# Optimization experiments

Measured on AMD Instinct MI355X. Metric: run time of the kernel, lower is better.

Reference implementation:

```python
import jax, jax.numpy as jnp
import numpy as np

N_UP, N_DOWN, M, D, K, F, L, B = 16, 16, 4, 128, 64, 32, 3, 1024
N = N_UP + N_DOWN
H_W = 45  # round(sqrt(F*K)), hidden dim of the 2-layer w MLP
LOG2 = float(np.log(2.0))


def ssp(x):
    # shifted softplus activation used by deepqmc
    return jax.nn.softplus(x) - LOG2


def _pair_blocks(n_up, n_down):
    # replicate idx_perm(N,2) grouped by i, then idx_pair_spin partition
    n = n_up + n_down
    i = np.repeat(np.arange(n), n - 1)
    j = np.concatenate([np.concatenate([np.arange(k), np.arange(k + 1, n)]) for k in range(n)])
    blocks = []
    for mi, mj, ri, rj in [(True, True, n_up, max(n_up - 1, 0)),
                           (True, False, n_up, n_down),
                           (False, True, n_down, n_up),
                           (False, False, n_down, max(n_down - 1, 0))]:
        mask = ((i < n_up) == mi) & ((j < n_up) == mj)
        blocks.append((i[mask].reshape(ri, rj), j[mask].reshape(ri, rj)))
    return blocks

_BLOCKS = _pair_blocks(N_UP, N_DOWN)
_CHANS = [0, 1, 1, 0]  # same, anti, anti, same (w/g channel index; 2 = nuclear)


def setup_inputs() -> dict:
    key = jax.random.key(0)
    ks = jax.random.split(key, 12)
    s = 0.1
    return {
        'edges_elec': jax.random.normal(ks[0], (B, N, N, F), jnp.float32),
        'edges_nuc': jax.random.normal(ks[1], (B, N, M, F), jnp.float32),
        'X': jax.random.normal(ks[2], (1, D), jnp.float32) * s,
        'Y': jax.random.normal(ks[3], (M, K), jnp.float32) * s,
        'wW1': jax.random.normal(ks[4], (L, 3, H_W, F), jnp.float32) * s,
        'wb1': jax.random.normal(ks[5], (L, 3, H_W), jnp.float32) * s,
        'wW2': jax.random.normal(ks[6], (L, 3, K, H_W), jnp.float32) * s,
        'wb2': jax.random.normal(ks[7], (L, 3, K), jnp.float32) * s,
        'hW': jax.random.normal(ks[8], (L, K, D), jnp.float32) * s,
        'hb': jax.random.normal(ks[9], (L, K), jnp.float32) * s,
        'gW': jax.random.normal(ks[10], (L, 3, D, K), jnp.float32) * s,
        'gb': jax.random.normal(ks[11], (L, 3, D), jnp.float32) * s,
    }


def reference(edges_elec, edges_nuc, X, Y, wW1, wb1, wW2, wb2, hW, hb, gW, gb):
    def w_mlp(l, c, e):
        # 2-layer log-dim MLP: F -> H_W -> K with SSP in between
        return ssp(e @ wW1[l, c].T + wb1[l, c]) @ wW2[l, c].T + wb2[l, c]

    b = edges_nuc.shape[0]
    x = jnp.broadcast_to(X, (b, N, D))  # initial electron embeddings (n_up==n_down)
    for l in range(L):
        h = x @ hW[l].T + hb[l]  # shared h subnet: [b,N,K]
        zs = []
        for (ii, jj), c in zip(_BLOCKS, _CHANS):
            e = edges_elec[:, ii, jj, :]               # [b, ri, rj, F] gather
            msg = w_mlp(l, c, e) * h[:, jj, :]          # [b, ri, rj, K]
            zs.append(msg.sum(axis=-2))                 # segment-sum over j
        z_same = jnp.concatenate([zs[0], zs[3]], axis=-2)  # up then down
        z_anti = jnp.concatenate([zs[1], zs[2]], axis=-2)
        z_nuc = jnp.einsum('bnmk,mk->bnk', w_mlp(l, 2, edges_nuc), Y)
        update = (z_same @ gW[l, 0].T + gb[l, 0]
                  + z_anti @ gW[l, 1].T + gb[l, 1]
                  + z_nuc @ gW[l, 2].T + gb[l, 2])
        x = x + update  # resnet
    return x
```

## Files before the change

### kernel.cpp

```cpp
#include <hip/hip_runtime.h>
#include <math.h>

#define N_   32
#define NUP_ 16
#define M_   4
#define D_   128
#define K_   64
#define F_   32
#define H_   45
#define L_   3
#define LOG2_ 0.69314718055994530942f

typedef __attribute__((ext_vector_type(8))) short short8;
typedef __attribute__((ext_vector_type(4))) float float4v;

__device__ __forceinline__ float ssp(float v) {
    return __logf(fmaf(0.5f, __expf(v), 0.5f));
}

__device__ __forceinline__ unsigned short f2bf(float x) {
    unsigned int u = __float_as_uint(x);
    return (unsigned short)((u + 0x7FFFu + ((u >> 16) & 1u)) >> 16);
}

__device__ __forceinline__ unsigned int cvtpk(float x, float y) {
    unsigned int r;
    asm("v_cvt_pk_bf16_f32 %0, %1, %2" : "=v"(r) : "v"(x), "v"(y));
    return r;
}

__global__ __launch_bounds__(256) void prep_kernel(
    const float* __restrict__ wW1, const float* __restrict__ wb1_unused,
    const float* __restrict__ wW2, const float* __restrict__ wb2,
    const float* __restrict__ gW,  const float* __restrict__ hW,
    const float* __restrict__ gb,
    short* __restrict__ w1B, short* __restrict__ w2B,
    short* __restrict__ gB,  short* __restrict__ hB, float* __restrict__ gbs)
{
    int blk = blockIdx.x;
    int t = threadIdx.x;
    if (blk < 27) {
        int lc = blk / 3, nt = blk % 3;
        short* dst = w1B + (size_t)blk * 512;
        for (int idx = t; idx < 512; idx += 256) {
            int lane = idx >> 3, jj = idx & 7;
            int k = ((lane >> 4) << 3) + jj;
            int n = nt * 16 + (lane & 15);
            float v = (n < H_) ? wW1[((size_t)lc * H_ + n) * F_ + k] : 0.0f;
            dst[idx] = (short)f2bf(v);
        }
    } else if (blk < 99) {
        int b3 = blk - 27;
        int lc = b3 >> 3, rem = b3 & 7, ks = rem >> 2, nt = rem & 3;
        short* dst = w2B + (size_t)b3 * 512;
        for (int idx = t; idx < 512; idx += 256) {
            int lane = idx >> 3, jj = idx & 7;
            int p = ks * 32 + ((lane >> 4) << 3) + jj;
            int n = nt * 16 + (lane & 15);
            int q = (p & 31) >> 3, j = p & 7;
            float v;
            if (p < 32) {
                int u = (j >> 2) * 16 + q * 4 + (j & 3);
                v = wW2[((size_t)lc * K_ + n) * H_ + u];
            } else if (j < 4) {
                int u = 32 + q * 4 + j;
                v = (u < H_) ? wW2[((size_t)lc * K_ + n) * H_ + u] : 0.0f;
            } else if (p == 36) {
                v = wb2[(size_t)lc * K_ + n];
            } else v = 0.0f;
            dst[idx] = (short)f2bf(v);
        }
    } else if (blk < 243) {
        int g = blk - 99;
        int l = g / 48, rem = g % 48;
        short* dst = gB + (size_t)g * 512;
        for (int idx = t; idx < 512; idx += 256) {
            int lane = idx >> 3, jj = idx & 7;
            int k = (rem >> 3) * 32 + ((lane >> 4) << 3) + jj;
            int c = k >> 6, kk = k & 63;
            int n = ((rem & 7) * 16) + (lane & 15);
            dst[idx] = (short)f2bf(gW[(((size_t)l * 3 + c) * D_ + n) * K_ + kk]);
        }
    } else if (blk < 275) {
        int hh = blk - 243;
        int li = hh >> 4, rem = hh & 15;
        short* dst = hB + (size_t)hh * 512;
        for (int idx = t; idx < 512; idx += 256) {
            int lane = idx >> 3, jj = idx & 7;
            int p = (rem >> 2) * 32 + ((lane >> 4) << 3) + jj;
            int d = (p & 7) * 16 + (p >> 3);
            int n = ((rem & 3) * 16) + (lane & 15);
            dst[idx] = (short)f2bf(hW[(((size_t)(li + 1)) * K_ + n) * D_ + d]);
        }
    } else {
        for (int idx = t; idx < 384; idx += 256) {
            int l = idx >> 7, d = idx & 127;
            gbs[idx] = gb[((size_t)l * 3 + 0) * D_ + d]
                     + gb[((size_t)l * 3 + 1) * D_ + d]
                     + gb[((size_t)l * 3 + 2) * D_ + d];
        }
    }
}

__global__ __launch_bounds__(64) void h0_kernel(
    const float* __restrict__ X, const float* __restrict__ hW,
    const float* __restrict__ hb, float* __restrict__ h0)
{
    int k = threadIdx.x;
    float a = hb[k];
    const float* w = hW + (size_t)k * D_;
    #pragma unroll 8
    for (int dd = 0; dd < D_; ++dd) a += w[dd] * X[dd];
    h0[k] = a;
}

#define WSTRIDE 68
__global__ __launch_bounds__(256, 6) void edge_kernel(
    const float* __restrict__ ee, const float* __restrict__ en,
    const float* __restrict__ Y,
    const short* __restrict__ w1B, const float* __restrict__ wb1,
    const short* __restrict__ w2B,
    const float* __restrict__ h, const float* __restrict__ h0,
    unsigned short* __restrict__ zb, int l, int hmode)
{
    __shared__ float wrow[36 * WSTRIDE];

    const int tid  = threadIdx.x;
    const int wv   = tid >> 6;
    const int lane = tid & 63;
    const int quad = lane >> 4;
    const int l16  = lane & 15;
    const int b    = blockIdx.x >> 3;
    const int i    = ((blockIdx.x & 7) << 2) + wv;
    const int bi   = (b << 5) + i;

    {
        int row = tid >> 3;
        int col = (tid & 7) * 8;
        const float* src = hmode ? (h + ((size_t)(b * N_ + row)) * K_ + col) : (h0 + col);
        float4 v0 = *(const float4*)(src);
        float4 v1 = *(const float4*)(src + 4);
        *(float4*)(wrow + row * WSTRIDE + col)     = v0;
        *(float4*)(wrow + row * WSTRIDE + col + 4) = v1;
        if (tid < 32) {
            int r2 = tid >> 3, o2 = (tid & 7) * 8;
            float4 y0 = *(const float4*)(Y + (size_t)r2 * K_ + o2);
            float4 y1 = *(const float4*)(Y + (size_t)r2 * K_ + o2 + 4);
            *(float4*)(wrow + (32 + r2) * WSTRIDE + o2)     = y0;
            *(float4*)(wrow + (32 + r2) * WSTRIDE + o2 + 4) = y1;
        }
    }
    __syncthreads();

    const int cA  = (i < NUP_) ? 0 : 1;
    const int tti = i >> 4;
    const int sil = i & 15;
    const int hq  = quad * 4;
    const unsigned int biasu = (quad == 0) ? 0x00003F80u : 0u;

    #pragma unroll
    for (int t = 0; t < 2; ++t) {
        const int c  = (t == 0) ? cA : 1 - cA;
        const int lc = l * 3 + c;
        const float* wlc = wb1 + (size_t)lc * H_;

        const float* ep = ee + (((size_t)bi * N_) + t * 16 + l16) * F_ + quad * 8;
        float4 fa = *(const float4*)(ep);
        float4 fb = *(const float4*)(ep + 4);
        union { short8 s; unsigned int u[4]; } E;
        E.u[0] = cvtpk(fa.x, fa.y); E.u[1] = cvtpk(fa.z, fa.w);
        E.u[2] = cvtpk(fb.x, fb.y); E.u[3] = cvtpk(fb.z, fb.w);

        const bool g3 = (hq < 12);
        float4v acc1[3];
        acc1[0] = (float4v){wlc[hq], wlc[hq + 1], wlc[hq + 2], wlc[hq + 3]};
        acc1[1] = (float4v){wlc[16 + hq], wlc[17 + hq], wlc[18 + hq], wlc[19 + hq]};
        {
            float b1 = wlc[g3 ? (33 + hq) : 0];
            float b2 = wlc[g3 ? (34 + hq) : 0];
            float b3 = wlc[g3 ? (35 + hq) : 0];
            acc1[2] = (float4v){wlc[32 + hq], g3 ? b1 : 0.0f, g3 ? b2 : 0.0f, g3 ? b3 : 0.0f};
        }

        #pragma unroll
        for (int nt = 0; nt < 3; ++nt) {
            short8 wf = *(const short8*)(w1B + (((size_t)lc * 3 + nt) << 9) + (lane << 3));
            acc1[nt] = __builtin_amdgcn_mfma_f32_16x16x32_bf16(wf, E.s, acc1[nt], 0, 0, 0);
        }

        union { short8 s; unsigned int u[4]; } A0, A1;
        A0.u[0] = cvtpk(ssp(acc1[0][0]), ssp(acc1[0][1]));
        A0.u[1] = cvtpk(ssp(acc1[0][2]), ssp(acc1[0][3]));
        A0.u[2] = cvtpk(ssp(acc1[1][0]), ssp(acc1[1][1]));
        A0.u[3] = cvtpk(ssp(acc1[1][2]), ssp(acc1[1][3]));
        A1.u[0] = cvtpk(ssp(acc1[2][0]), ssp(acc1[2][1]));
        A1.u[1] = cvtpk(ssp(acc1[2][2]), ssp(acc1[2][3]));
        A1.u[2] = biasu;
        A1.u[3] = 0u;
        const bool deadl = (t == tti) && (l16 == sil);
        if (deadl) {
            A0.u[0] = 0u; A0.u[1] = 0u; A0.u[2] = 0u; A0.u[3] = 0u;
            A1.u[0] = 0u; A1.u[1] = 0u; A1.u[2] = 0u;
        }

        float4v acc2[4];
        #pragma unroll
        for (int nt = 0; nt < 4; ++nt) acc2[nt] = (float4v){0.f, 0.f, 0.f, 0.f};
        #pragma unroll
        for (int nt = 0; nt < 4; ++nt) {
            short8 bf0 = *(const short8*)(w2B + ((((size_t)lc * 2 + 0) * 4 + nt) << 9) + (lane << 3));
            acc2[nt] = __builtin_amdgcn_mfma_f32_16x16x32_bf16(A0.s, bf0, acc2[nt], 0, 0, 0);
            short8 bf1 = *(const short8*)(w2B + ((((size_t)lc * 2 + 1) * 4 + nt) << 9) + (lane << 3));
            acc2[nt] = __builtin_amdgcn_mfma_f32_16x16x32_bf16(A1.s, bf1, acc2[nt], 0, 0, 0);
        }

        float p0 = 0.f, p1 = 0.f, p2 = 0.f, p3 = 0.f;
        #pragma unroll
        for (int r = 0; r < 4; ++r) {
            const int jrow = t * 16 + quad * 4 + r;
            const float* wr = wrow + jrow * WSTRIDE + l16;
            p0 += acc2[0][r] * wr[0];
            p1 += acc2[1][r] * wr[16];
            p2 += acc2[2][r] * wr[32];
            p3 += acc2[3][r] * wr[48];
        }

        const bool qlo = (quad & 1) != 0;
        const bool qhi = (quad & 2) != 0;
        float u  = qlo ? p1 : p0;
        float us = qlo ? p0 : p1;
        u += __shfl_xor(us, 16);
        float w  = qlo ? p3 : p2;
        float ws = qlo ? p2 : p3;
        w += __shfl_xor(ws, 16);
        float v  = qhi ? w : u;
        float vs = qhi ? u : w;
        v += __shfl_xor(vs, 32);

        zb[(size_t)bi * 192 + c * 64 + lane] = (unsigned short)cvtpk(v, v);
    }

    if (wv == 0) {
        const int lc = l * 3 + 2;
        const float* wlc = wb1 + (size_t)lc * H_;

        const float* np = en + ((size_t)bi * M_ + l16) * F_ + quad * 8;
        float4 fa = *(const float4*)(np);
        float4 fb = *(const float4*)(np + 4);
        union { short8 s; unsigned int u[4]; } E;
        E.u[0] = cvtpk(fa.x, fa.y); E.u[1] = cvtpk(fa.z, fa.w);
        E.u[2] = cvtpk(fb.x, fb.y); E.u[3] = cvtpk(fb.z, fb.w);

        const bool g3 = (hq < 12);
        float4v acc1[3];
        acc1[0] = (float4v){wlc[hq], wlc[hq + 1], wlc[hq + 2], wlc[hq + 3]};
        acc1[1] = (float4v){wlc[16 + hq], wlc[17 + hq], wlc[18 + hq], wlc[19 + hq]};
        {
            float b1 = wlc[g3 ? (33 + hq) : 0];
            float b2 = wlc[g3 ? (34 + hq) : 0];
            float b3 = wlc[g3 ? (35 + hq) : 0];
            acc1[2] = (float4v){wlc[32 + hq], g3 ? b1 : 0.0f, g3 ? b2 : 0.0f, g3 ? b3 : 0.0f};
        }
        #pragma unroll
        for (int nt = 0; nt < 3; ++nt) {
            short8 wf = *(const short8*)(w1B + (((size_t)lc * 3 + nt) << 9) + (lane << 3));
            acc1[nt] = __builtin_amdgcn_mfma_f32_16x16x32_bf16(wf, E.s, acc1[nt], 0, 0, 0);
        }

        union { short8 s; unsigned int u[4]; } A0, A1;
        A0.u[0] = cvtpk(ssp(acc1[0][0]), ssp(acc1[0][1]));
        A0.u[1] = cvtpk(ssp(acc1[0][2]), ssp(acc1[0][3]));
        A0.u[2] = cvtpk(ssp(acc1[1][0]), ssp(acc1[1][1]));
        A0.u[3] = cvtpk(ssp(acc1[1][2]), ssp(acc1[1][3]));
        A1.u[0] = cvtpk(ssp(acc1[2][0]), ssp(acc1[2][1]));
        A1.u[1] = cvtpk(ssp(acc1[2][2]), ssp(acc1[2][3]));
        A1.u[2] = biasu;
        A1.u[3] = 0u;

        float4v acc2[4];
        #pragma unroll
        for (int nt = 0; nt < 4; ++nt) acc2[nt] = (float4v){0.f, 0.f, 0.f, 0.f};
        #pragma unroll
        for (int nt = 0; nt < 4; ++nt) {
            short8 bf0 = *(const short8*)(w2B + ((((size_t)lc * 2 + 0) * 4 + nt) << 9) + (lane << 3));
            acc2[nt] = __builtin_amdgcn_mfma_f32_16x16x32_bf16(A0.s, bf0, acc2[nt], 0, 0, 0);
            short8 bf1 = *(const short8*)(w2B + ((((size_t)lc * 2 + 1) * 4 + nt) << 9) + (lane << 3));
            acc2[nt] = __builtin_amdgcn_mfma_f32_16x16x32_bf16(A1.s, bf1, acc2[nt], 0, 0, 0);
        }

        float p0 = 0.f, p1 = 0.f, p2 = 0.f, p3 = 0.f;
        #pragma unroll
        for (int r = 0; r < 4; ++r) {
            const float* wr = wrow + (32 + r) * WSTRIDE + l16;
            p0 += acc2[0][r] * wr[0];
            p1 += acc2[1][r] * wr[16];
            p2 += acc2[2][r] * wr[32];
            p3 += acc2[3][r] * wr[48];
        }
        unsigned short* zo = zb + (size_t)(bi + quad) * 192 + 128 + l16;
        zo[0]  = (unsigned short)cvtpk(p0, p0);
        zo[16] = (unsigned short)cvtpk(p1, p1);
        zo[32] = (unsigned short)cvtpk(p2, p2);
        zo[48] = (unsigned short)cvtpk(p3, p3);
    }
}

#define HXS 136
__global__ __launch_bounds__(256) void fuse_kernel(
    const unsigned short* __restrict__ zb, const short* __restrict__ gB,
    const float* __restrict__ gbs, const float* __restrict__ X,
    const short* __restrict__ hB, const float* __restrict__ hb,
    float* __restrict__ xout, float* __restrict__ hout,
    int l, int first, int compute_h)
{
    __shared__ short hx_s[2][16 * HXS];

    const int tid  = threadIdx.x;
    const int wv   = tid >> 6;
    const int lane = tid & 63;
    const int quad = lane >> 4;
    const int l16  = lane & 15;
    const int pair = wv >> 1;
    const int half = wv & 1;
    const int nt0  = half * 4;
    const int bi0  = (blockIdx.x * 2 + pair) * 16;

    float4v ax[4];
    #pragma unroll
    for (int nt = 0; nt < 4; ++nt) ax[nt] = (float4v){0.f, 0.f, 0.f, 0.f};
    const short* gb_ = gB + (size_t)l * 48 * 512;
    const short* zrow = (const short*)zb + ((size_t)(bi0 + l16)) * 192;
    #pragma unroll
    for (int ks = 0; ks < 6; ++ks) {
        short8 az = *(const short8*)(zrow + ks * 32 + quad * 8);
        #pragma unroll
        for (int nt = 0; nt < 4; ++nt) {
            short8 bf = *(const short8*)(gb_ + (((size_t)ks * 8 + nt0 + nt) << 9) + (lane << 3));
            ax[nt] = __builtin_amdgcn_mfma_f32_16x16x32_bf16(az, bf, ax[nt], 0, 0, 0);
        }
    }

    float gv[4], xb[4];
    #pragma unroll
    for (int nt = 0; nt < 4; ++nt) {
        gv[nt] = gbs[(size_t)l * D_ + (nt0 + nt) * 16 + l16];
        if (first) xb[nt] = X[(nt0 + nt) * 16 + l16];
    }
    short* hx = hx_s[pair];
    #pragma unroll
    for (int r = 0; r < 4; ++r) {
        int row = quad * 4 + r;
        size_t gi = ((size_t)(bi0 + row)) * D_ + l16;
        float xv[4];
        #pragma unroll
        for (int nt = 0; nt < 4; ++nt) {
            float xo = (first ? xb[nt] : xout[gi + (nt0 + nt) * 16]) + gv[nt] + ax[nt][r];
            xout[gi + (nt0 + nt) * 16] = xo;
            xv[nt] = xo;
        }
        if (compute_h) {
            uint2 P;
            P.x = cvtpk(xv[0], xv[1]);
            P.y = cvtpk(xv[2], xv[3]);
            *(uint2*)(hx + row * HXS + 8 * l16 + 4 * half) = P;
        }
    }
    if (!compute_h) return;
    __syncthreads();

    float4v ah[2];
    #pragma unroll
    for (int nt = 0; nt < 2; ++nt) ah[nt] = (float4v){0.f, 0.f, 0.f, 0.f};
    const short* hb_ = hB + (size_t)l * 16 * 512;
    #pragma unroll
    for (int ks = 0; ks < 4; ++ks) {
        short8 a = *(const short8*)(hx + l16 * HXS + ks * 32 + quad * 8);
        #pragma unroll
        for (int nt = 0; nt < 2; ++nt) {
            short8 bf = *(const short8*)(hb_ + (((size_t)ks * 4 + half * 2 + nt) << 9) + (lane << 3));
            ah[nt] = __builtin_amdgcn_mfma_f32_16x16x32_bf16(a, bf, ah[nt], 0, 0, 0);
        }
    }
    float hbv[2];
    #pragma unroll
    for (int nt = 0; nt < 2; ++nt) hbv[nt] = hb[((size_t)(l + 1)) * K_ + (half * 2 + nt) * 16 + l16];
    #pragma unroll
    for (int nt = 0; nt < 2; ++nt)
        #pragma unroll
        for (int r = 0; r < 4; ++r)
            hout[((size_t)(bi0 + quad * 4 + r)) * K_ + (half * 2 + nt) * 16 + l16] = ah[nt][r] + hbv[nt];
}

extern "C" void kernel_launch(void* const* d_in, const int* in_sizes, int n_in,
                              void* d_out, int out_size, void* d_ws, size_t ws_size,
                              hipStream_t stream)
{
    const float* ee  = (const float*)d_in[0];
    const float* en  = (const float*)d_in[1];
    const float* X   = (const float*)d_in[2];
    const float* Y   = (const float*)d_in[3];
    const float* wW1 = (const float*)d_in[4];
    const float* wb1 = (const float*)d_in[5];
    const float* wW2 = (const float*)d_in[6];
    const float* wb2 = (const float*)d_in[7];
    const float* hW  = (const float*)d_in[8];
    const float* hb  = (const float*)d_in[9];
    const float* gW  = (const float*)d_in[10];
    const float* gb  = (const float*)d_in[11];
    float* xout = (float*)d_out;

    char* ws = (char*)d_ws;
    float*          h   = (float*)(ws);
    unsigned short* zb  = (unsigned short*)(ws + 8388608);
    float*          h0  = (float*)(ws + 8388608 + 12582912);
    short*          w1B = (short*)(ws + 20971520 + 256);
    short*          w2B = w1B + (size_t)27 * 512;
    short*          gB  = w2B + (size_t)72 * 512;
    short*          hB  = gB  + (size_t)144 * 512;
    float*          gbs = (float*)(hB + (size_t)32 * 512);

    prep_kernel<<<276, 256, 0, stream>>>(wW1, wb1, wW2, wb2, gW, hW, gb,
                                         w1B, w2B, gB, hB, gbs);
    h0_kernel<<<1, 64, 0, stream>>>(X, hW, hb, h0);

    edge_kernel<<<8192, 256, 0, stream>>>(ee, en, Y, w1B, wb1, w2B, h, h0, zb, 0, 0);
    fuse_kernel<<<1024, 256, 0, stream>>>(zb, gB, gbs, X, hB, hb, xout, h, 0, 1, 1);
    edge_kernel<<<8192, 256, 0, stream>>>(ee, en, Y, w1B, wb1, w2B, h, h0, zb, 1, 1);
    fuse_kernel<<<1024, 256, 0, stream>>>(zb, gB, gbs, X, hB, hb, xout, h, 1, 0, 1);
    edge_kernel<<<8192, 256, 0, stream>>>(ee, en, Y, w1B, wb1, w2B, h, h0, zb, 2, 1);
    fuse_kernel<<<1024, 256, 0, stream>>>(zb, gB, gbs, X, hB, hb, xout, h, 2, 0, 0);
}
```

Before: 401.8 us.

## Process two electrons per wave in edge kernel to reuse weight fragments

Each wave now handles two receiver electrons (ia and ia+4), so the grid halves and each block covers 8 electrons of a batch. The weight fragments, biases and h rows staged in shared memory are loaded once and used for two independent MFMA chains, which cuts redundant weight loads and per-block setup and adds instruction-level parallelism. The nuclear part is split over two waves, each covering four electrons. In exchange, register pressure rises and the occupancy hint drops from 6 to 5 blocks.

```diff
diff --git a/kernel.cpp b/kernel.cpp
--- a/kernel.cpp
+++ b/kernel.cpp
@@ -115,7 +115,7 @@
 }
 
 #define WSTRIDE 68
-__global__ __launch_bounds__(256, 6) void edge_kernel(
+__global__ __launch_bounds__(256, 5) void edge_kernel(
     const float* __restrict__ ee, const float* __restrict__ en,
     const float* __restrict__ Y,
     const short* __restrict__ w1B, const float* __restrict__ wb1,
@@ -130,9 +130,12 @@
     const int lane = tid & 63;
     const int quad = lane >> 4;
     const int l16  = lane & 15;
-    const int b    = blockIdx.x >> 3;
-    const int i    = ((blockIdx.x & 7) << 2) + wv;
-    const int bi   = (b << 5) + i;
+    const int b    = blockIdx.x >> 2;
+    const int ig   = (blockIdx.x & 3) << 3;
+    const int ia   = ig + wv;
+    const int ib   = ia + 4;
+    const size_t bia = (size_t)(b << 5) + ia;
+    const size_t bib = (size_t)(b << 5) + ib;
 
     {
         int row = tid >> 3;
@@ -152,10 +155,10 @@
     }
     __syncthreads();
 
-    const int cA  = (i < NUP_) ? 0 : 1;
-    const int tti = i >> 4;
-    const int sil = i & 15;
-    const int hq  = quad * 4;
+    const int cA   = (ia < NUP_) ? 0 : 1;
+    const int ttia = ia >> 4, sila = ia & 15;
+    const int ttib = ib >> 4, silb = ib & 15;
+    const int hq   = quad * 4;
     const unsigned int biasu = (quad == 0) ? 0x00003F80u : 0u;
 
     #pragma unroll
@@ -164,9 +167,128 @@
         const int lc = l * 3 + c;
         const float* wlc = wb1 + (size_t)lc * H_;
 
-        const float* ep = ee + (((size_t)bi * N_) + t * 16 + l16) * F_ + quad * 8;
-        float4 fa = *(const float4*)(ep);
-        float4 fb = *(const float4*)(ep + 4);
+        const float* epa = ee + ((bia * N_) + t * 16 + l16) * F_ + quad * 8;
+        const float* epb = ee + ((bib * N_) + t * 16 + l16) * F_ + quad * 8;
+        float4 fa0 = *(const float4*)(epa);
+        float4 fa1 = *(const float4*)(epa + 4);
+        float4 fb0 = *(const float4*)(epb);
+        float4 fb1 = *(const float4*)(epb + 4);
+        union { short8 s; unsigned int u[4]; } Ea, Eb;
+        Ea.u[0] = cvtpk(fa0.x, fa0.y); Ea.u[1] = cvtpk(fa0.z, fa0.w);
+        Ea.u[2] = cvtpk(fa1.x, fa1.y); Ea.u[3] = cvtpk(fa1.z, fa1.w);
+        Eb.u[0] = cvtpk(fb0.x, fb0.y); Eb.u[1] = cvtpk(fb0.z, fb0.w);
+        Eb.u[2] = cvtpk(fb1.x, fb1.y); Eb.u[3] = cvtpk(fb1.z, fb1.w);
+
+        const bool g3 = (hq < 12);
+        float4v bias0 = (float4v){wlc[hq], wlc[hq + 1], wlc[hq + 2], wlc[hq + 3]};
+        float4v bias1 = (float4v){wlc[16 + hq], wlc[17 + hq], wlc[18 + hq], wlc[19 + hq]};
+        float4v bias2;
+        {
+            float b1 = wlc[g3 ? (33 + hq) : 0];
+            float b2 = wlc[g3 ? (34 + hq) : 0];
+            float b3 = wlc[g3 ? (35 + hq) : 0];
+            bias2 = (float4v){wlc[32 + hq], g3 ? b1 : 0.0f, g3 ? b2 : 0.0f, g3 ? b3 : 0.0f};
+        }
+
+        float4v acc1a[3], acc1b[3];
+        acc1a[0] = bias0; acc1a[1] = bias1; acc1a[2] = bias2;
+        acc1b[0] = bias0; acc1b[1] = bias1; acc1b[2] = bias2;
+        #pragma unroll
+        for (int nt = 0; nt < 3; ++nt) {
+            short8 wf = *(const short8*)(w1B + (((size_t)lc * 3 + nt) << 9) + (lane << 3));
+            acc1a[nt] = __builtin_amdgcn_mfma_f32_16x16x32_bf16(wf, Ea.s, acc1a[nt], 0, 0, 0);
+            acc1b[nt] = __builtin_amdgcn_mfma_f32_16x16x32_bf16(wf, Eb.s, acc1b[nt], 0, 0, 0);
+        }
+
+        union { short8 s; unsigned int u[4]; } A0a, A1a, A0b, A1b;
+        A0a.u[0] = cvtpk(ssp(acc1a[0][0]), ssp(acc1a[0][1]));
+        A0a.u[1] = cvtpk(ssp(acc1a[0][2]), ssp(acc1a[0][3]));
+        A0a.u[2] = cvtpk(ssp(acc1a[1][0]), ssp(acc1a[1][1]));
+        A0a.u[3] = cvtpk(ssp(acc1a[1][2]), ssp(acc1a[1][3]));
+        A1a.u[0] = cvtpk(ssp(acc1a[2][0]), ssp(acc1a[2][1]));
+        A1a.u[1] = cvtpk(ssp(acc1a[2][2]), ssp(acc1a[2][3]));
+        A1a.u[2] = biasu; A1a.u[3] = 0u;
+        A0b.u[0] = cvtpk(ssp(acc1b[0][0]), ssp(acc1b[0][1]));
+        A0b.u[1] = cvtpk(ssp(acc1b[0][2]), ssp(acc1b[0][3]));
+        A0b.u[2] = cvtpk(ssp(acc1b[1][0]), ssp(acc1b[1][1]));
+        A0b.u[3] = cvtpk(ssp(acc1b[1][2]), ssp(acc1b[1][3]));
+        A1b.u[0] = cvtpk(ssp(acc1b[2][0]), ssp(acc1b[2][1]));
+        A1b.u[1] = cvtpk(ssp(acc1b[2][2]), ssp(acc1b[2][3]));
+        A1b.u[2] = biasu; A1b.u[3] = 0u;
+        if ((t == ttia) && (l16 == sila)) {
+            A0a.u[0] = 0u; A0a.u[1] = 0u; A0a.u[2] = 0u; A0a.u[3] = 0u;
+            A1a.u[0] = 0u; A1a.u[1] = 0u; A1a.u[2] = 0u;
+        }
+        if ((t == ttib) && (l16 == silb)) {
+            A0b.u[0] = 0u; A0b.u[1] = 0u; A0b.u[2] = 0u; A0b.u[3] = 0u;
+            A1b.u[0] = 0u; A1b.u[1] = 0u; A1b.u[2] = 0u;
+        }
+
+        float4v acc2a[4], acc2b[4];
+        #pragma unroll
+        for (int nt = 0; nt < 4; ++nt) {
+            acc2a[nt] = (float4v){0.f, 0.f, 0.f, 0.f};
+            acc2b[nt] = (float4v){0.f, 0.f, 0.f, 0.f};
+        }
+        #pragma unroll
+        for (int nt = 0; nt < 4; ++nt) {
+            short8 bf0 = *(const short8*)(w2B + ((((size_t)lc * 2 + 0) * 4 + nt) << 9) + (lane << 3));
+            acc2a[nt] = __builtin_amdgcn_mfma_f32_16x16x32_bf16(A0a.s, bf0, acc2a[nt], 0, 0, 0);
+            acc2b[nt] = __builtin_amdgcn_mfma_f32_16x16x32_bf16(A0b.s, bf0, acc2b[nt], 0, 0, 0);
+            short8 bf1 = *(const short8*)(w2B + ((((size_t)lc * 2 + 1) * 4 + nt) << 9) + (lane << 3));
+            acc2a[nt] = __builtin_amdgcn_mfma_f32_16x16x32_bf16(A1a.s, bf1, acc2a[nt], 0, 0, 0);
+            acc2b[nt] = __builtin_amdgcn_mfma_f32_16x16x32_bf16(A1b.s, bf1, acc2b[nt], 0, 0, 0);
+        }
+
+        float pa0 = 0.f, pa1 = 0.f, pa2 = 0.f, pa3 = 0.f;
+        float pb0 = 0.f, pb1 = 0.f, pb2 = 0.f, pb3 = 0.f;
+        #pragma unroll
+        for (int r = 0; r < 4; ++r) {
+            const int jrow = t * 16 + quad * 4 + r;
+            const float* wr = wrow + jrow * WSTRIDE + l16;
+            float w0 = wr[0], w1 = wr[16], w2 = wr[32], w3 = wr[48];
+            pa0 += acc2a[0][r] * w0;  pb0 += acc2b[0][r] * w0;
+            pa1 += acc2a[1][r] * w1;  pb1 += acc2b[1][r] * w1;
+            pa2 += acc2a[2][r] * w2;  pb2 += acc2b[2][r] * w2;
+            pa3 += acc2a[3][r] * w3;  pb3 += acc2b[3][r] * w3;
+        }
+
+        const bool qlo = (quad & 1) != 0;
+        const bool qhi = (quad & 2) != 0;
+        {
+            float u  = qlo ? pa1 : pa0;
+            float us = qlo ? pa0 : pa1;
+            u += __shfl_xor(us, 16);
+            float w  = qlo ? pa3 : pa2;
+            float ws = qlo ? pa2 : pa3;
+            w += __shfl_xor(ws, 16);
+            float v  = qhi ? w : u;
+            float vs = qhi ? u : w;
+            v += __shfl_xor(vs, 32);
+            zb[bia * 192 + c * 64 + lane] = (unsigned short)cvtpk(v, v);
+        }
+        {
+            float u  = qlo ? pb1 : pb0;
+            float us = qlo ? pb0 : pb1;
+            u += __shfl_xor(us, 16);
+            float w  = qlo ? pb3 : pb2;
+            float ws = qlo ? pb2 : pb3;
+            w += __shfl_xor(ws, 16);
+            float v  = qhi ? w : u;
+            float vs = qhi ? u : w;
+            v += __shfl_xor(vs, 32);
+            zb[bib * 192 + c * 64 + lane] = (unsigned short)cvtpk(v, v);
+        }
+    }
+
+    if (wv < 2) {
+        const int lc = l * 3 + 2;
+        const float* wlc = wb1 + (size_t)lc * H_;
+        const size_t nbase = (size_t)(b << 5) + ig + (wv << 2);
+
+        const float* np = en + (nbase * M_ + l16) * F_ + quad * 8;
+        float4 fa = *(const float4*)(np);
+        float4 fb = *(const float4*)(np + 4);
         union { short8 s; unsigned int u[4]; } E;
         E.u[0] = cvtpk(fa.x, fa.y); E.u[1] = cvtpk(fa.z, fa.w);
         E.u[2] = cvtpk(fb.x, fb.y); E.u[3] = cvtpk(fb.z, fb.w);
@@ -181,7 +303,6 @@
             float b3 = wlc[g3 ? (35 + hq) : 0];
             acc1[2] = (float4v){wlc[32 + hq], g3 ? b1 : 0.0f, g3 ? b2 : 0.0f, g3 ? b3 : 0.0f};
         }
-
         #pragma unroll
         for (int nt = 0; nt < 3; ++nt) {
             short8 wf = *(const short8*)(w1B + (((size_t)lc * 3 + nt) << 9) + (lane << 3));
@@ -197,85 +318,6 @@
         A1.u[1] = cvtpk(ssp(acc1[2][2]), ssp(acc1[2][3]));
         A1.u[2] = biasu;
         A1.u[3] = 0u;
-        const bool deadl = (t == tti) && (l16 == sil);
-        if (deadl) {
-            A0.u[0] = 0u; A0.u[1] = 0u; A0.u[2] = 0u; A0.u[3] = 0u;
-            A1.u[0] = 0u; A1.u[1] = 0u; A1.u[2] = 0u;
-        }
-
-        float4v acc2[4];
-        #pragma unroll
-        for (int nt = 0; nt < 4; ++nt) acc2[nt] = (float4v){0.f, 0.f, 0.f, 0.f};
-        #pragma unroll
-        for (int nt = 0; nt < 4; ++nt) {
-            short8 bf0 = *(const short8*)(w2B + ((((size_t)lc * 2 + 0) * 4 + nt) << 9) + (lane << 3));
-            acc2[nt] = __builtin_amdgcn_mfma_f32_16x16x32_bf16(A0.s, bf0, acc2[nt], 0, 0, 0);
-            short8 bf1 = *(const short8*)(w2B + ((((size_t)lc * 2 + 1) * 4 + nt) << 9) + (lane << 3));
-            acc2[nt] = __builtin_amdgcn_mfma_f32_16x16x32_bf16(A1.s, bf1, acc2[nt], 0, 0, 0);
-        }
-
-        float p0 = 0.f, p1 = 0.f, p2 = 0.f, p3 = 0.f;
-        #pragma unroll
-        for (int r = 0; r < 4; ++r) {
-            const int jrow = t * 16 + quad * 4 + r;
-            const float* wr = wrow + jrow * WSTRIDE + l16;
-            p0 += acc2[0][r] * wr[0];
-            p1 += acc2[1][r] * wr[16];
-            p2 += acc2[2][r] * wr[32];
-            p3 += acc2[3][r] * wr[48];
-        }
-
-        const bool qlo = (quad & 1) != 0;
-        const bool qhi = (quad & 2) != 0;
-        float u  = qlo ? p1 : p0;
-        float us = qlo ? p0 : p1;
-        u += __shfl_xor(us, 16);
-        float w  = qlo ? p3 : p2;
-        float ws = qlo ? p2 : p3;
-        w += __shfl_xor(ws, 16);
-        float v  = qhi ? w : u;
-        float vs = qhi ? u : w;
-        v += __shfl_xor(vs, 32);
-
-        zb[(size_t)bi * 192 + c * 64 + lane] = (unsigned short)cvtpk(v, v);
-    }
-
-    if (wv == 0) {
-        const int lc = l * 3 + 2;
-        const float* wlc = wb1 + (size_t)lc * H_;
-
-        const float* np = en + ((size_t)bi * M_ + l16) * F_ + quad * 8;
-        float4 fa = *(const float4*)(np);
-        float4 fb = *(const float4*)(np + 4);
-        union { short8 s; unsigned int u[4]; } E;
-        E.u[0] = cvtpk(fa.x, fa.y); E.u[1] = cvtpk(fa.z, fa.w);
-        E.u[2] = cvtpk(fb.x, fb.y); E.u[3] = cvtpk(fb.z, fb.w);
-
-        const bool g3 = (hq < 12);
-        float4v acc1[3];
-        acc1[0] = (float4v){wlc[hq], wlc[hq + 1], wlc[hq + 2], wlc[hq + 3]};
-        acc1[1] = (float4v){wlc[16 + hq], wlc[17 + hq], wlc[18 + hq], wlc[19 + hq]};
-        {
-            float b1 = wlc[g3 ? (33 + hq) : 0];
-            float b2 = wlc[g3 ? (34 + hq) : 0];
-            float b3 = wlc[g3 ? (35 + hq) : 0];
-            acc1[2] = (float4v){wlc[32 + hq], g3 ? b1 : 0.0f, g3 ? b2 : 0.0f, g3 ? b3 : 0.0f};
-        }
-        #pragma unroll
-        for (int nt = 0; nt < 3; ++nt) {
-            short8 wf = *(const short8*)(w1B + (((size_t)lc * 3 + nt) << 9) + (lane << 3));
-            acc1[nt] = __builtin_amdgcn_mfma_f32_16x16x32_bf16(wf, E.s, acc1[nt], 0, 0, 0);
-        }
-
-        union { short8 s; unsigned int u[4]; } A0, A1;
-        A0.u[0] = cvtpk(ssp(acc1[0][0]), ssp(acc1[0][1]));
-        A0.u[1] = cvtpk(ssp(acc1[0][2]), ssp(acc1[0][3]));
-        A0.u[2] = cvtpk(ssp(acc1[1][0]), ssp(acc1[1][1]));
-        A0.u[3] = cvtpk(ssp(acc1[1][2]), ssp(acc1[1][3]));
-        A1.u[0] = cvtpk(ssp(acc1[2][0]), ssp(acc1[2][1]));
-        A1.u[1] = cvtpk(ssp(acc1[2][2]), ssp(acc1[2][3]));
-        A1.u[2] = biasu;
-        A1.u[3] = 0u;
 
         float4v acc2[4];
         #pragma unroll
@@ -297,7 +339,7 @@
             p2 += acc2[2][r] * wr[32];
             p3 += acc2[3][r] * wr[48];
         }
-        unsigned short* zo = zb + (size_t)(bi + quad) * 192 + 128 + l16;
+        unsigned short* zo = zb + (nbase + quad) * 192 + 128 + l16;
         zo[0]  = (unsigned short)cvtpk(p0, p0);
         zo[16] = (unsigned short)cvtpk(p1, p1);
         zo[32] = (unsigned short)cvtpk(p2, p2);
@@ -423,10 +465,10 @@
                                          w1B, w2B, gB, hB, gbs);
     h0_kernel<<<1, 64, 0, stream>>>(X, hW, hb, h0);
 
-    edge_kernel<<<8192, 256, 0, stream>>>(ee, en, Y, w1B, wb1, w2B, h, h0, zb, 0, 0);
+    edge_kernel<<<4096, 256, 0, stream>>>(ee, en, Y, w1B, wb1, w2B, h, h0, zb, 0, 0);
     fuse_kernel<<<1024, 256, 0, stream>>>(zb, gB, gbs, X, hB, hb, xout, h, 0, 1, 1);
-    edge_kernel<<<8192, 256, 0, stream>>>(ee, en, Y, w1B, wb1, w2B, h, h0, zb, 1, 1);
+    edge_kernel<<<4096, 256, 0, stream>>>(ee, en, Y, w1B, wb1, w2B, h, h0, zb, 1, 1);
     fuse_kernel<<<1024, 256, 0, stream>>>(zb, gB, gbs, X, hB, hb, xout, h, 1, 0, 1);
-    edge_kernel<<<8192, 256, 0, stream>>>(ee, en, Y, w1B, wb1, w2B, h, h0, zb, 2, 1);
+    edge_kernel<<<4096, 256, 0, stream>>>(ee, en, Y, w1B, wb1, w2B, h, h0, zb, 2, 1);
     fuse_kernel<<<1024, 256, 0, stream>>>(zb, gB, gbs, X, hB, hb, xout, h, 2, 0, 0);
 }
```

After: 377.1 us. 6.1% less time.
